# Kernel tuning notes

Hardware: AMD Instinct MI355X
Metric: run time of the kernel (lower is better)

The kernel has to match this reference:

```python
import jax, jax.numpy as jnp
import numpy as np

EPS = 1e-5  # BatchNorm eps; eval-mode BN with running_mean=0, running_var=1 -> affine


def pe3d(C, x, y, z):
    """PositionalEncoding3D -> (C, x, y, z), faithfully reproducing the torch
    broadcasting (emb_x of shape (x,1,c) assigned into (x,y,z,c) slices)."""
    c = int(np.ceil(C / 3))
    inv_freq = jnp.asarray(1.0 / (10000.0 ** (np.arange(0, c, 2, dtype=np.float32) / c)))
    def emb(n):
        s = jnp.arange(n, dtype=jnp.float32)[:, None] * inv_freq[None, :]
        return jnp.concatenate([jnp.sin(s), jnp.cos(s)], axis=-1)  # (n, c)
    ex = emb(x)[:, None, :]   # (x,1,c) -> broadcasts as (1,x,1,c), same as torch
    ey = emb(y)[:, None, :]   # (y,1,c)
    ez = emb(z)               # (z,c)
    out = jnp.zeros((x, y, z, 3 * c), dtype=jnp.float32)
    out = out.at[..., :c].set(ex)
    out = out.at[..., c:2 * c].set(ey)
    out = out.at[..., 2 * c:3 * c].set(ez)
    return jnp.transpose(out[..., :C], (3, 0, 1, 2))  # (C,x,y,z)


def conv1x1(x, w, b):  # x:(B,Ci,D,H,W) w:(Co,Ci)
    return jnp.einsum('bcdhw,oc->bodhw', x, w) + b[None, :, None, None, None]


def bn_relu(x, g, b):  # eval BN (mean 0, var 1) + ReLU
    s = g / jnp.sqrt(1.0 + EPS)
    return jax.nn.relu(x * s[None, :, None, None, None] + b[None, :, None, None, None])


def setup_inputs() -> dict:
    key = jax.random.key(0)
    ks = jax.random.split(key, 16)
    B, Cy, Cs, D, H, W = 2, 96, 48, 16, 16, 16
    w = lambda k, shp: jax.random.normal(k, shp, dtype=jnp.float32) * 0.05
    return {
        'Y': jax.random.normal(ks[0], (B, Cy, D, H, W), dtype=jnp.float32),
        'S': jax.random.normal(ks[1], (B, Cs, D, H, W), dtype=jnp.float32),
        'w_s': w(ks[2], (Cs, Cs)), 'b_s': jnp.zeros((Cs,), jnp.float32),
        'g_s': jnp.ones((Cs,), jnp.float32), 'be_s': jnp.zeros((Cs,), jnp.float32),
        'w_y': w(ks[3], (Cs, Cy)), 'b_y': jnp.zeros((Cs,), jnp.float32),
        'g_y': jnp.ones((Cs,), jnp.float32), 'be_y': jnp.zeros((Cs,), jnp.float32),
        'Wq': w(ks[4], (Cs, Cs)), 'Wk': w(ks[5], (Cs, Cs)), 'Wv': w(ks[6], (Cs, Cs)),
        'w_o': w(ks[7], (Cs, Cs)), 'b_o': jnp.zeros((Cs,), jnp.float32),
        'g_o': jnp.ones((Cs,), jnp.float32), 'be_o': jnp.zeros((Cs,), jnp.float32),
        'w3': w(ks[8], (Cy, Cy, 3, 3, 3)), 'b3': jnp.zeros((Cy,), jnp.float32),
        'w_y2': w(ks[9], (Cs, Cy)), 'b_y2': jnp.zeros((Cs,), jnp.float32),
        'g_y2': jnp.ones((Cs,), jnp.float32), 'be_y2': jnp.zeros((Cs,), jnp.float32),
    }


def reference(Y, S, w_s, b_s, g_s, be_s, w_y, b_y, g_y, be_y, Wq, Wk, Wv,
              w_o, b_o, g_o, be_o, w3, b3, w_y2, b_y2, g_y2, be_y2):
    B, Cs, D, H, W = S.shape
    Cy = Y.shape[1]
    N = D * H * W
    # positional encodings (added, not learned)
    S = S + pe3d(Cs, D, H, W)[None]
    Y = Y + pe3d(Cy, D, H, W)[None]
    # projections: conv1x1 + BN + ReLU
    S1 = bn_relu(conv1x1(S, w_s, b_s), g_s, be_s).reshape(B, Cs, N).transpose(0, 2, 1)  # (B,N,Cs)
    Y1 = bn_relu(conv1x1(Y, w_y, b_y), g_y, be_y).reshape(B, Cs, N).transpose(0, 2, 1)  # (B,N,Cs)
    # Yconv2: 3x3x3 conv -> 1x1 conv -> BN -> ReLU
    Y3 = jax.lax.conv_general_dilated(Y, w3, (1, 1, 1), 'SAME',
                                      dimension_numbers=('NCDHW', 'OIDHW', 'NCDHW'))
    Y3 = Y3 + b3[None, :, None, None, None]
    Y2 = bn_relu(conv1x1(Y3, w_y2, b_y2), g_y2, be_y2)  # (B,Cs,D,H,W)
    # MultiHeadDense = plain right-matmul by (d,d) weight
    Q = jnp.einsum('bnd,de->bne', Y1, Wq)
    K = jnp.einsum('bnd,de->bne', Y1, Wk)
    V = jnp.einsum('bnd,de->bne', S1, Wv)
    # attention with NON-STANDARD softmax over axis=1 (queries, not keys)
    A = jax.nn.softmax(jnp.einsum('bqd,bkd->bqk', Q, K) * (float(Cs) ** -0.5), axis=1)
    x = jnp.einsum('bqk,bkd->bqd', A, V)                       # (B,N,Cs)
    x = x.transpose(0, 2, 1).reshape(B, Cs, D, H, W)
    Z = bn_relu(conv1x1(x, w_o, b_o), g_o, be_o) * S
    return jnp.concatenate([Z, Y2], axis=1)  # (B, 2*Cs, D, H, W)
```

## Files before the change

### kernel.cpp

```cpp
#include <hip/hip_runtime.h>
#include <hip/hip_bf16.h>

#define NPOS 4096
#define BB 2
#define KS2 32
#define QS2 32

typedef short v4s __attribute__((ext_vector_type(4)));
typedef short v8s __attribute__((ext_vector_type(8)));
typedef float v4f __attribute__((ext_vector_type(4)));
typedef unsigned short ushort_t;

static __device__ __forceinline__ unsigned short f2bf(float f) {
    unsigned int u = __float_as_uint(f);
    return (unsigned short)((u + 0x7fffu + ((u >> 16) & 1u)) >> 16);
}
static __device__ __forceinline__ float bf2f(ushort_t s) {
    return __uint_as_float(((unsigned int)s) << 16);
}

__device__ __forceinline__ float pe_val(int C, int c, int ch, int h, int w) {
    int blk = ch / c;
    int j = ch - blk * c;
    int half = c >> 1;
    int jj = (j < half) ? j : j - half;
    float freq = __expf(-(2.0f * jj / (float)c) * 9.210340371976184f);
    int pos = (blk < 2) ? h : w;
    float s = (float)pos * freq;
    return (j < half) ? __sinf(s) : __cosf(s);
}

__global__ void prep1_kernel(const float* __restrict__ S, const float* __restrict__ Y,
                             const float* __restrict__ w3, float* __restrict__ S_pe,
                             float* __restrict__ Y_pe, ushort_t* __restrict__ wr) {
    int bid = blockIdx.x;
    int t = threadIdx.x;
    __shared__ float tb[16];
    if (bid < 384) {
        int idx4 = bid * 256 + t;
        int ch = (idx4 >> 10) % 48;
        if (t < 16) tb[t] = pe_val(48, 16, ch, t, t);
        __syncthreads();
        int n = (idx4 & 1023) * 4;
        int h = (n >> 4) & 15, w0 = n & 15;
        v4f x = *(const v4f*)&S[(size_t)idx4 * 4];
        if (ch < 32) {
            float p = tb[h];
#pragma unroll
            for (int j = 0; j < 4; j++) x[j] += p;
        } else {
#pragma unroll
            for (int j = 0; j < 4; j++) x[j] += tb[w0 + j];
        }
        *(v4f*)&S_pe[(size_t)idx4 * 4] = x;
    } else if (bid < 1152) {
        int idx4 = (bid - 384) * 256 + t;
        int ch = (idx4 >> 10) % 96;
        if (t < 16) tb[t] = pe_val(96, 32, ch, t, t);
        __syncthreads();
        int n = (idx4 & 1023) * 4;
        int h = (n >> 4) & 15, w0 = n & 15;
        v4f x = *(const v4f*)&Y[(size_t)idx4 * 4];
        if (ch < 64) {
            float p = tb[h];
#pragma unroll
            for (int j = 0; j < 4; j++) x[j] += p;
        } else {
#pragma unroll
            for (int j = 0; j < 4; j++) x[j] += tb[w0 + j];
        }
        *(v4f*)&Y_pe[(size_t)idx4 * 4] = x;
    } else {
        int idx = (bid - 1152) * 256 + t;
        if (idx < 27 * 96 * 96) {
            int ci = idx % 96;
            int t2 = idx / 96;
            int co = t2 % 96;
            int tap = t2 / 96;
            wr[idx] = f2bf(w3[(size_t)(co * 96 + ci) * 27 + tap]);
        }
    }
}

template<int CI>
__device__ __forceinline__ void proj_body(int r, const float* __restrict__ in,
                                          const float* __restrict__ w, const float* __restrict__ bias,
                                          const float* __restrict__ g, const float* __restrict__ be,
                                          float* __restrict__ out) {
    int pc = r >> 3, cc = r & 7;
    int o0 = cc * 6;
    __shared__ float wl[6 * CI];
    __shared__ float sb[6], bb[6];
    int t = threadIdx.x;
    for (int i = t; i < 6 * CI; i += 256) {
        int o = i / CI, ci = i - o * CI;
        wl[i] = w[(size_t)(o0 + o) * CI + ci];
    }
    if (t < 6) {
        float s = g[o0 + t] * rsqrtf(1.0f + 1e-5f);
        sb[t] = s; bb[t] = bias[o0 + t] * s + be[o0 + t];
    }
    __syncthreads();
    int gn = pc * 256 + t;
    int b = gn >> 12;
    const float* ip = in + (size_t)b * CI * NPOS + (gn & 4095);
    float acc[6];
#pragma unroll
    for (int o = 0; o < 6; o++) acc[o] = 0.f;
#pragma unroll
    for (int ci = 0; ci < CI; ci++) {
        float v = ip[(size_t)ci * NPOS];
#pragma unroll
        for (int o = 0; o < 6; o++) acc[o] += v * wl[o * CI + ci];
    }
    float* op = out + (size_t)gn * 48 + o0;
#pragma unroll
    for (int o = 0; o < 6; o++) {
        float z = acc[o] * sb[o] + bb[o];
        op[o] = z > 0.f ? z : 0.f;
    }
}

__global__ void prep2_kernel(const float* __restrict__ Y_pe, const float* __restrict__ S_pe,
                             const float* __restrict__ w_s, const float* __restrict__ b_s,
                             const float* __restrict__ g_s, const float* __restrict__ be_s,
                             const float* __restrict__ w_y, const float* __restrict__ b_y,
                             const float* __restrict__ g_y, const float* __restrict__ be_y,
                             ushort_t* __restrict__ Ypad, float* __restrict__ S1,
                             float* __restrict__ Y1) {
    int bid = blockIdx.x;
    if (bid < 1094) {
        int idx = bid * 256 + threadIdx.x;
        if (idx >= BB * 5832 * 24) return;
        int ci4 = idx % 24;
        int cell = idx / 24;
        int wp = cell % 18; int c2 = cell / 18;
        int hp = c2 % 18; int c3 = c2 / 18;
        int zp = c3 % 18; int b = c3 / 18;
        ushort_t pk[4] = {0, 0, 0, 0};
        if (zp >= 1 && zp <= 16 && hp >= 1 && hp <= 16 && wp >= 1 && wp <= 16) {
            int n = (zp - 1) * 256 + (hp - 1) * 16 + (wp - 1);
#pragma unroll
            for (int j = 0; j < 4; j++)
                pk[j] = f2bf(Y_pe[((size_t)(b * 96 + ci4 * 4 + j) << 12) + n]);
        }
        *(v4s*)&Ypad[(size_t)idx * 4] = *(v4s*)pk;
    } else {
        int r = bid - 1094;
        if (r < 256) proj_body<48>(r, S_pe, w_s, b_s, g_s, be_s, S1);
        else proj_body<96>(r - 256, Y_pe, w_y, b_y, g_y, be_y, Y1);
    }
}

__global__ void qkv_kernel(const float* __restrict__ Y1, const float* __restrict__ S1,
                           const float* __restrict__ Wq, const float* __restrict__ Wk,
                           const float* __restrict__ Wv, ushort_t* __restrict__ Qb,
                           ushort_t* __restrict__ Kb, ushort_t* __restrict__ Vt) {
    int grp = blockIdx.x >> 8;
    int r = blockIdx.x & 255;
    int pc = r >> 3, cc = r & 7;
    int o0 = cc * 6;
    const float* in = (grp == 2) ? S1 : Y1;
    const float* w = (grp == 0) ? Wq : (grp == 1) ? Wk : Wv;
    __shared__ float wl[48 * 6];
    int t = threadIdx.x;
    for (int i = t; i < 48 * 6; i += 256) {
        int d = i / 6, o = i - d * 6;
        wl[i] = w[(size_t)d * 48 + o0 + o];
    }
    __syncthreads();
    int gn = pc * 256 + t;
    const float* ip = in + (size_t)gn * 48;
    float acc[6];
#pragma unroll
    for (int o = 0; o < 6; o++) acc[o] = 0.f;
#pragma unroll
    for (int d = 0; d < 48; d++) {
        float v = ip[d];
#pragma unroll
        for (int o = 0; o < 6; o++) acc[o] += v * wl[d * 6 + o];
    }
    if (grp < 2) {
        ushort_t* base = (grp == 0 ? Qb : Kb) + (size_t)gn * 64;
#pragma unroll
        for (int o = 0; o < 6; o++) base[o0 + o] = f2bf(acc[o]);
        if (cc == 0) {
            v8s z = {0, 0, 0, 0, 0, 0, 0, 0};
            *(v8s*)(base + 48) = z;
            *(v8s*)(base + 56) = z;
        }
    } else {
        int b = gn >> 12; int n = gn & 4095;
#pragma unroll
        for (int o = 0; o < 6; o++)
            Vt[((size_t)(b * 48 + o0 + o) << 12) + n] = f2bf(acc[o]);
    }
}

__global__ void attn_stats_mfma_kernel(const ushort_t* __restrict__ Qb,
                                       const ushort_t* __restrict__ Kb,
                                       float* __restrict__ ps) {
    int bid = blockIdx.x;
    int qs = bid & 31; int kb = (bid >> 5) & 15; int b = bid >> 9;
    int t = threadIdx.x; int wv = t >> 6; int lane = t & 63;
    int lr = lane & 15, g = lane >> 4;
    const float scale = 0.14433756729740643f;
    int key0 = kb * 256 + wv * 64;
    v8s ka[4][2];
#pragma unroll
    for (int kt = 0; kt < 4; kt++) {
        const ushort_t* krow = Kb + ((size_t)(b * NPOS + key0 + kt * 16 + lr)) * 64;
        ka[kt][0] = *(const v8s*)(krow + 8 * g);
        ka[kt][1] = *(const v8s*)(krow + 32 + 8 * g);
    }
    float s[4][4];
#pragma unroll
    for (int kt = 0; kt < 4; kt++)
#pragma unroll
        for (int r = 0; r < 4; r++) s[kt][r] = 0.f;
    for (int qt = 0; qt < 8; qt++) {
        int q = qs * 128 + qt * 16 + lr;
        const ushort_t* qrow = Qb + ((size_t)(b * NPOS + q)) * 64;
        v8s qf0 = *(const v8s*)(qrow + 8 * g);
        v8s qf1 = *(const v8s*)(qrow + 32 + 8 * g);
#pragma unroll
        for (int kt = 0; kt < 4; kt++) {
            v4f acc = {0.f, 0.f, 0.f, 0.f};
            acc = __builtin_amdgcn_mfma_f32_16x16x32_bf16(ka[kt][0], qf0, acc, 0, 0, 0);
            acc = __builtin_amdgcn_mfma_f32_16x16x32_bf16(ka[kt][1], qf1, acc, 0, 0, 0);
#pragma unroll
            for (int r = 0; r < 4; r++) s[kt][r] += __expf(acc[r] * scale);
        }
    }
#pragma unroll
    for (int off = 1; off < 16; off <<= 1)
#pragma unroll
        for (int kt = 0; kt < 4; kt++)
#pragma unroll
            for (int r = 0; r < 4; r++) s[kt][r] += __shfl_xor(s[kt][r], off);
    if (lr == 0) {
#pragma unroll
        for (int kt = 0; kt < 4; kt++) {
            int idx = (b * QS2 + qs) * NPOS + key0 + kt * 16 + 4 * g;
            v4f ss = {s[kt][0], s[kt][1], s[kt][2], s[kt][3]};
            *(v4f*)&ps[idx] = ss;
        }
    }
}

__global__ void norm_vscale_kernel(const float* __restrict__ ps, ushort_t* __restrict__ Vt) {
    int idx = blockIdx.x * 256 + threadIdx.x;
    if (idx >= BB * 4 * NPOS) return;
    int k = idx & 4095;
    int rest = idx >> 12;
    int dg = rest & 3; int b = rest >> 2;
    float s = 0.f;
#pragma unroll
    for (int qs = 0; qs < QS2; qs++) s += ps[(size_t)(b * QS2 + qs) * NPOS + k];
    float ci = 1.0f / s;
#pragma unroll
    for (int d = dg * 12; d < dg * 12 + 12; d++) {
        size_t a = ((size_t)(b * 48 + d) << 12) + k;
        Vt[a] = f2bf(bf2f(Vt[a]) * ci);
    }
}

__device__ __forceinline__ void pv_body(int bid, const ushort_t* __restrict__ Qb,
                                        const ushort_t* __restrict__ Kb,
                                        const ushort_t* __restrict__ Vt,
                                        ushort_t* __restrict__ xpart) {
    int ks = bid & 31; int qb = (bid >> 5) & 15; int b = bid >> 9;
    int t = threadIdx.x; int wv = t >> 6; int lane = t & 63;
    int lr = lane & 15, g = lane >> 4;
    const float scale = 0.14433756729740643f;
    int q0 = qb * 256 + wv * 64;
    v8s qf[4][2];
#pragma unroll
    for (int qt = 0; qt < 4; qt++) {
        const ushort_t* qrow = Qb + ((size_t)(b * NPOS + q0 + qt * 16 + lr)) * 64;
        qf[qt][0] = *(const v8s*)(qrow + 8 * g);
        qf[qt][1] = *(const v8s*)(qrow + 32 + 8 * g);
    }
    v4f xacc[4][3];
#pragma unroll
    for (int qt = 0; qt < 4; qt++)
#pragma unroll
        for (int nt = 0; nt < 3; nt++) xacc[qt][nt] = (v4f){0.f, 0.f, 0.f, 0.f};
    for (int kt = 0; kt < 2; kt++) {
        int kb0 = ks * 128 + kt * 64;
        v4s p[4][4];
#pragma unroll
        for (int tm = 0; tm < 4; tm++) {
            const ushort_t* krow = Kb + ((size_t)(b * NPOS + kb0 + 16 * tm + lr)) * 64;
            v8s ka0 = *(const v8s*)(krow + 8 * g);
            v8s ka1 = *(const v8s*)(krow + 32 + 8 * g);
#pragma unroll
            for (int qt = 0; qt < 4; qt++) {
                v4f acc = {0.f, 0.f, 0.f, 0.f};
                acc = __builtin_amdgcn_mfma_f32_16x16x32_bf16(ka0, qf[qt][0], acc, 0, 0, 0);
                acc = __builtin_amdgcn_mfma_f32_16x16x32_bf16(ka1, qf[qt][1], acc, 0, 0, 0);
                v4s pp;
#pragma unroll
                for (int r = 0; r < 4; r++)
                    pp[r] = (short)f2bf(__expf(acc[r] * scale));
                p[tm][qt] = pp;
            }
        }
#pragma unroll
        for (int nt = 0; nt < 3; nt++) {
            const ushort_t* vrow = Vt + ((size_t)(b * 48 + 16 * nt + lr) << 12) + kb0;
#pragma unroll
            for (int tm = 0; tm < 4; tm++) {
                v4s vf = *(const v4s*)(vrow + 16 * tm + 4 * g);
#pragma unroll
                for (int qt = 0; qt < 4; qt++)
                    xacc[qt][nt] = __builtin_amdgcn_mfma_f32_16x16x16bf16_1k(
                        p[tm][qt], vf, xacc[qt][nt], 0, 0, 0);
            }
        }
    }
#pragma unroll
    for (int qt = 0; qt < 4; qt++)
#pragma unroll
        for (int nt = 0; nt < 3; nt++)
#pragma unroll
            for (int r = 0; r < 4; r++)
                xpart[(((size_t)(b * KS2 + ks) << 12) + q0 + qt * 16 + 4 * g + r) * 48 + 16 * nt + lr] =
                    f2bf(xacc[qt][nt][r]);
}

__device__ __forceinline__ void conv_body(int bid, const ushort_t* __restrict__ Ypad,
                                          const ushort_t* __restrict__ wr,
                                          const float* __restrict__ b3,
                                          float* __restrict__ Y3) {
    int b = bid / 384;
    int r = bid % 384;
    int cot = r % 6;
    int zhq = r / 6;
    int t = threadIdx.x; int wv = t >> 6; int lane = t & 63;
    int z = zhq >> 2;
    int h = (zhq & 3) * 4 + wv;
    int lr = lane & 15, g = lane >> 4;
    v4f acc[3];
#pragma unroll
    for (int kd = 0; kd < 3; kd++) acc[kd] = (v4f){0.f, 0.f, 0.f, 0.f};
    const ushort_t* wbase = wr + (size_t)(cot * 16 + lr) * 96 + 8 * g;
#pragma unroll
    for (int kd = 0; kd < 3; kd++) {
#pragma unroll
        for (int kh = 0; kh < 3; kh++) {
            const ushort_t* arow = Ypad + (((size_t)(b * 18 + z + kd) * 18 + h + kh) * 18 + lr) * 96 + 8 * g;
            int tap0 = (kd * 3 + kh) * 3;
            v8s af[3][3], bf[3][3];
#pragma unroll
            for (int kw = 0; kw < 3; kw++)
#pragma unroll
                for (int c = 0; c < 3; c++) {
                    af[kw][c] = *(const v8s*)(arow + kw * 96 + c * 32);
                    bf[kw][c] = *(const v8s*)(wbase + (size_t)(tap0 + kw) * 96 * 96 + c * 32);
                }
#pragma unroll
            for (int kw = 0; kw < 3; kw++)
#pragma unroll
                for (int c = 0; c < 3; c++)
                    acc[kd] = __builtin_amdgcn_mfma_f32_16x16x32_bf16(
                        af[kw][c], bf[kw][c], acc[kd], 0, 0, 0);
        }
    }
    float bv = b3[cot * 16 + lr];
    int pos = z * 256 + h * 16 + 4 * g;
#pragma unroll
    for (int r2 = 0; r2 < 4; r2++)
        Y3[(((size_t)b << 12) + pos + r2) * 96 + cot * 16 + lr] =
            acc[0][r2] + acc[1][r2] + acc[2][r2] + bv;
}

__global__ __launch_bounds__(256, 2)
void pvconv_kernel(const ushort_t* __restrict__ Qb, const ushort_t* __restrict__ Kb,
                   const ushort_t* __restrict__ Vt, ushort_t* __restrict__ xpart,
                   const ushort_t* __restrict__ Ypad, const ushort_t* __restrict__ wr,
                   const float* __restrict__ b3, float* __restrict__ Y3) {
    int bid = blockIdx.x;
    if (bid < BB * 16 * KS2) pv_body(bid, Qb, Kb, Vt, xpart);
    else conv_body(bid - BB * 16 * KS2, Ypad, wr, b3, Y3);
}

__global__ void xreduce_kernel(const ushort_t* __restrict__ xpart, float* __restrict__ xsum) {
    int v = blockIdx.x * 256 + threadIdx.x;
    if (v >= BB * NPOS * 6) return;
    int b = v / (NPOS * 6);
    int rem8 = (v - b * NPOS * 6) * 8;
    float s[8];
#pragma unroll
    for (int j = 0; j < 8; j++) s[j] = 0.f;
    const ushort_t* base = xpart + (size_t)b * KS2 * NPOS * 48 + rem8;
#pragma unroll 4
    for (int ks = 0; ks < KS2; ks++) {
        v8s x = *(const v8s*)(base + (size_t)ks * NPOS * 48);
#pragma unroll
        for (int j = 0; j < 8; j++) s[j] += bf2f((ushort_t)x[j]);
    }
    float* op = xsum + (size_t)b * NPOS * 48 + rem8;
    v4f lo = {s[0], s[1], s[2], s[3]};
    v4f hi = {s[4], s[5], s[6], s[7]};
    *(v4f*)op = lo;
    *(v4f*)(op + 4) = hi;
}

__device__ __forceinline__ void z_out_body(int r, const float* __restrict__ xsum,
                                           const float* __restrict__ w_o, const float* __restrict__ b_o,
                                           const float* __restrict__ g_o, const float* __restrict__ be_o,
                                           const float* __restrict__ S_pe, float* __restrict__ out) {
    int pc = r >> 3, cc = r & 7;
    int o0 = cc * 6;
    __shared__ float wl[6 * 48];
    __shared__ float sb[6], bb[6];
    int t = threadIdx.x;
    for (int i = t; i < 6 * 48; i += 256) {
        int o = i / 48, d = i - o * 48;
        wl[i] = w_o[(size_t)(o0 + o) * 48 + d];
    }
    if (t < 6) {
        float s = g_o[o0 + t] * rsqrtf(1.f + 1e-5f);
        sb[t] = s; bb[t] = b_o[o0 + t] * s + be_o[o0 + t];
    }
    __syncthreads();
    int gn = pc * 256 + t;
    int b = gn >> 12; int n = gn & 4095;
    const v4f* p = (const v4f*)(xsum + (size_t)gn * 48);
    float x[48];
#pragma unroll
    for (int d4 = 0; d4 < 12; d4++) {
        v4f v = p[d4];
#pragma unroll
        for (int j = 0; j < 4; j++) x[d4 * 4 + j] = v[j];
    }
#pragma unroll
    for (int o = 0; o < 6; o++) {
        float acc = 0.f;
#pragma unroll
        for (int d = 0; d < 48; d++) acc += wl[o * 48 + d] * x[d];
        float z = acc * sb[o] + bb[o];
        z = z > 0.f ? z : 0.f;
        out[((size_t)b * 96 + o0 + o) * NPOS + n] = z * S_pe[((size_t)b * 48 + o0 + o) * NPOS + n];
    }
}

__device__ __forceinline__ void y2_out_body(int r, const float* __restrict__ Y3,
                                            const float* __restrict__ w_y2, const float* __restrict__ b_y2,
                                            const float* __restrict__ g_y2, const float* __restrict__ be_y2,
                                            float* __restrict__ out) {
    int pc = r >> 3, cc = r & 7;
    int o0 = cc * 6;
    __shared__ float wl2[6 * 96];
    __shared__ float sb2[6], bb2[6];
    int t = threadIdx.x;
    for (int i = t; i < 6 * 96; i += 256) {
        int o = i / 96, ci = i - o * 96;
        wl2[i] = w_y2[(size_t)(o0 + o) * 96 + ci];
    }
    if (t < 6) {
        float s = g_y2[o0 + t] * rsqrtf(1.f + 1e-5f);
        sb2[t] = s; bb2[t] = b_y2[o0 + t] * s + be_y2[o0 + t];
    }
    __syncthreads();
    int gn = pc * 256 + t;
    int b = gn >> 12; int n = gn & 4095;
    const v4f* ip = (const v4f*)(Y3 + (size_t)gn * 96);
    float acc[6];
#pragma unroll
    for (int o = 0; o < 6; o++) acc[o] = 0.f;
#pragma unroll
    for (int c4 = 0; c4 < 24; c4++) {
        v4f v = ip[c4];
#pragma unroll
        for (int j = 0; j < 4; j++)
#pragma unroll
            for (int o = 0; o < 6; o++) acc[o] += v[j] * wl2[o * 96 + c4 * 4 + j];
    }
#pragma unroll
    for (int o = 0; o < 6; o++) {
        float z = acc[o] * sb2[o] + bb2[o];
        out[((size_t)b * 96 + 48 + o0 + o) * NPOS + n] = z > 0.f ? z : 0.f;
    }
}

__global__ void zy_out_kernel(const float* __restrict__ xsum, const float* __restrict__ w_o,
                              const float* __restrict__ b_o, const float* __restrict__ g_o,
                              const float* __restrict__ be_o, const float* __restrict__ S_pe,
                              const float* __restrict__ Y3, const float* __restrict__ w_y2,
                              const float* __restrict__ b_y2, const float* __restrict__ g_y2,
                              const float* __restrict__ be_y2, float* __restrict__ out) {
    int bid = blockIdx.x;
    if (bid < 256) z_out_body(bid, xsum, w_o, b_o, g_o, be_o, S_pe, out);
    else y2_out_body(bid - 256, Y3, w_y2, b_y2, g_y2, be_y2, out);
}

extern "C" void kernel_launch(void* const* d_in, const int* in_sizes, int n_in,
                              void* d_out, int out_size, void* d_ws, size_t ws_size,
                              hipStream_t stream) {
    const float* Y    = (const float*)d_in[0];
    const float* S    = (const float*)d_in[1];
    const float* w_s  = (const float*)d_in[2];
    const float* b_s  = (const float*)d_in[3];
    const float* g_s  = (const float*)d_in[4];
    const float* be_s = (const float*)d_in[5];
    const float* w_y  = (const float*)d_in[6];
    const float* b_y  = (const float*)d_in[7];
    const float* g_y  = (const float*)d_in[8];
    const float* be_y = (const float*)d_in[9];
    const float* Wq   = (const float*)d_in[10];
    const float* Wk   = (const float*)d_in[11];
    const float* Wv   = (const float*)d_in[12];
    const float* w_o  = (const float*)d_in[13];
    const float* b_o  = (const float*)d_in[14];
    const float* g_o  = (const float*)d_in[15];
    const float* be_o = (const float*)d_in[16];
    const float* w3   = (const float*)d_in[17];
    const float* b3   = (const float*)d_in[18];
    const float* w_y2 = (const float*)d_in[19];
    const float* b_y2 = (const float*)d_in[20];
    const float* g_y2 = (const float*)d_in[21];
    const float* be_y2= (const float*)d_in[22];
    float* out = (float*)d_out;

    float* ws = (float*)d_ws;
    float* S_pe   = ws;
    float* Y_pe   = ws + 393216;
    float* S1     = ws + 1179648;
    float* Y1     = ws + 1572864;
    ushort_t* Qb  = (ushort_t*)(ws + 1966080);
    ushort_t* Kb  = (ushort_t*)(ws + 2228224);
    ushort_t* Vt  = (ushort_t*)(ws + 2490368);
    float* ps     = ws + 2686976;
    ushort_t* xpart = (ushort_t*)(ws + 2949120);
    float* xsum   = ws + 9240576;
    float* Y3     = ws + 9633792;
    ushort_t* Ypad= (ushort_t*)(ws + 10420224);
    ushort_t* wr  = (ushort_t*)(ws + 10980096);

    prep1_kernel<<<2124, 256, 0, stream>>>(S, Y, w3, S_pe, Y_pe, wr);
    prep2_kernel<<<1606, 256, 0, stream>>>(Y_pe, S_pe, w_s, b_s, g_s, be_s,
                                           w_y, b_y, g_y, be_y, Ypad, S1, Y1);
    qkv_kernel<<<768, 256, 0, stream>>>(Y1, S1, Wq, Wk, Wv, Qb, Kb, Vt);
    attn_stats_mfma_kernel<<<BB * 16 * QS2, 256, 0, stream>>>(Qb, Kb, ps);
    norm_vscale_kernel<<<128, 256, 0, stream>>>(ps, Vt);
    pvconv_kernel<<<BB * 16 * KS2 + 768, 256, 0, stream>>>(Qb, Kb, Vt, xpart,
                                                           Ypad, wr, b3, Y3);
    xreduce_kernel<<<192, 256, 0, stream>>>(xpart, xsum);
    zy_out_kernel<<<512, 256, 0, stream>>>(xsum, w_o, b_o, g_o, be_o, S_pe,
                                           Y3, w_y2, b_y2, g_y2, be_y2, out);
}
```

Baseline: 136.9 us.

## Stage K and V tiles in swizzled LDS and interleave PV/conv blocks

The PV attention body now loads its 128-key K tile and V slice into shared memory once per block, using an XOR swizzle to avoid bank conflicts. The four waves then read from LDS instead of each fetching the same K/V rows from global memory. The block-index mapping also interleaves attention and conv blocks in a 4:3 ratio so the two workloads mix across CUs instead of running back to back. The cost is extra LDS use (about 28 KB per block), which may lower occupancy, plus one added barrier. The interleave assumes the conv block count divides evenly into the 4:3 pattern.

Result: faster. 133.9 us (-2.2%).

```diff
diff --git a/kernel.cpp b/kernel.cpp
--- a/kernel.cpp
+++ b/kernel.cpp
@@ -269,10 +269,27 @@
                                         const ushort_t* __restrict__ Kb,
                                         const ushort_t* __restrict__ Vt,
                                         ushort_t* __restrict__ xpart) {
+    __shared__ ushort_t Kl[128 * 64];
+    __shared__ ushort_t Vl[48 * 128];
     int ks = bid & 31; int qb = (bid >> 5) & 15; int b = bid >> 9;
     int t = threadIdx.x; int wv = t >> 6; int lane = t & 63;
     int lr = lane & 15, g = lane >> 4;
     const float scale = 0.14433756729740643f;
+    int kb0 = ks * 128;
+    {
+        const ushort_t* src = Kb + ((size_t)(b * NPOS + kb0)) * 64;
+        for (int i = t; i < 1024; i += 256) {
+            int row = i >> 3, slot = i & 7;
+            *(v8s*)&Kl[row * 64 + ((slot ^ (row & 7)) << 3)] =
+                *(const v8s*)(src + row * 64 + slot * 8);
+        }
+        const ushort_t* vsrc = Vt + ((size_t)(b * 48) << 12) + kb0;
+        for (int i = t; i < 1536; i += 256) {
+            int row = i >> 5, s8 = i & 31;
+            *(v4s*)&Vl[row * 128 + ((s8 ^ (row & 15)) << 2)] =
+                *(const v4s*)(vsrc + ((size_t)row << 12) + s8 * 4);
+        }
+    }
     int q0 = qb * 256 + wv * 64;
     v8s qf[4][2];
 #pragma unroll
@@ -281,19 +298,19 @@
         qf[qt][0] = *(const v8s*)(qrow + 8 * g);
         qf[qt][1] = *(const v8s*)(qrow + 32 + 8 * g);
     }
+    __syncthreads();
     v4f xacc[4][3];
 #pragma unroll
     for (int qt = 0; qt < 4; qt++)
 #pragma unroll
         for (int nt = 0; nt < 3; nt++) xacc[qt][nt] = (v4f){0.f, 0.f, 0.f, 0.f};
     for (int kt = 0; kt < 2; kt++) {
-        int kb0 = ks * 128 + kt * 64;
         v4s p[4][4];
 #pragma unroll
         for (int tm = 0; tm < 4; tm++) {
-            const ushort_t* krow = Kb + ((size_t)(b * NPOS + kb0 + 16 * tm + lr)) * 64;
-            v8s ka0 = *(const v8s*)(krow + 8 * g);
-            v8s ka1 = *(const v8s*)(krow + 32 + 8 * g);
+            int krow = kt * 64 + 16 * tm + lr;
+            v8s ka0 = *(const v8s*)&Kl[krow * 64 + ((g ^ (krow & 7)) << 3)];
+            v8s ka1 = *(const v8s*)&Kl[krow * 64 + (((4 + g) ^ (krow & 7)) << 3)];
 #pragma unroll
             for (int qt = 0; qt < 4; qt++) {
                 v4f acc = {0.f, 0.f, 0.f, 0.f};
@@ -308,10 +325,11 @@
         }
 #pragma unroll
         for (int nt = 0; nt < 3; nt++) {
-            const ushort_t* vrow = Vt + ((size_t)(b * 48 + 16 * nt + lr) << 12) + kb0;
 #pragma unroll
             for (int tm = 0; tm < 4; tm++) {
-                v4s vf = *(const v4s*)(vrow + 16 * tm + 4 * g);
+                int vrowd = 16 * nt + lr;
+                int s8 = 16 * kt + 4 * tm + g;
+                v4s vf = *(const v4s*)&Vl[vrowd * 128 + ((s8 ^ (vrowd & 15)) << 2)];
 #pragma unroll
                 for (int qt = 0; qt < 4; qt++)
                     xacc[qt][nt] = __builtin_amdgcn_mfma_f32_16x16x16bf16_1k(
@@ -380,9 +398,9 @@
                    const ushort_t* __restrict__ Vt, ushort_t* __restrict__ xpart,
                    const ushort_t* __restrict__ Ypad, const ushort_t* __restrict__ wr,
                    const float* __restrict__ b3, float* __restrict__ Y3) {
-    int bid = blockIdx.x;
-    if (bid < BB * 16 * KS2) pv_body(bid, Qb, Kb, Vt, xpart);
-    else conv_body(bid - BB * 16 * KS2, Ypad, wr, b3, Y3);
+    int g7 = blockIdx.x / 7, r7 = blockIdx.x % 7;
+    if (r7 < 4) pv_body(g7 * 4 + r7, Qb, Kb, Vt, xpart);
+    else conv_body(g7 * 3 + (r7 - 4), Ypad, wr, b3, Y3);
 }
 
 __global__ void xreduce_kernel(const ushort_t* __restrict__ xpart, float* __restrict__ xsum) {
```
